# Optimization experiments

Hardware: AMD Instinct MI355X
Metric: run time of the kernel (lower is better)

Reference implementation:

```python
import jax, jax.numpy as jnp
import numpy as np
from jax import lax

C_IN, N_BR, K, H, W_IMG, B = 16, 32, 5, 224, 224, 16
C_SEL = C_IN // 2  # each pattern column selects exactly 8 channels
# circulant connectivity pattern, matches init_kwargs pattern literal
PATTERN = ((np.arange(C_IN)[:, None] + np.arange(N_BR)[None, :]) % C_IN < C_SEL).astype(np.int64)
# np.where returns sorted indices, matching the torch forward's index order
IDX = np.stack([np.where(PATTERN[:, i] == 1)[0] for i in range(N_BR)])  # [N_BR, C_SEL]


def setup_inputs() -> dict:
    key = jax.random.key(0)
    k1, k2, k3 = jax.random.split(key, 3)
    x = jax.random.normal(k1, (B, C_IN, H, W_IMG), dtype=jnp.float32)
    # per-branch conv weights stacked: branch i has Conv2d(8 -> 1, 5x5)
    Wc = jax.random.normal(k2, (N_BR, C_SEL, K, K), dtype=jnp.float32) * 0.05
    bc = jax.random.normal(k3, (N_BR,), dtype=jnp.float32) * 0.05
    return {"x": x, "Wc": Wc, "bc": bc}


def reference(x, Wc, bc):
    # gather the selected channels for every branch: [B, N_BR*C_SEL, H, W]
    x_sel = x[:, IDX.reshape(-1)]
    # all branches at once as a grouped convolution (groups = N_BR, 1 out/group)
    y = lax.conv_general_dilated(
        x_sel, Wc,
        window_strides=(1, 1),
        padding=[(2, 2), (2, 2)],
        feature_group_count=N_BR,
        dimension_numbers=("NCHW", "OIHW", "NCHW"),
    )  # [B, N_BR, H, W]
    return jax.nn.sigmoid(y + bc[None, :, None, None])
```

## Files before the change

kernel.cpp:

```cpp
#include <hip/hip_runtime.h>
#include <math.h>


#define HH 224
#define WW 224
#define BB 16
#define CIN 16
#define NBR 32
#define PH 228
#define PW 228
#define KSTEPS 13

typedef short short8 __attribute__((ext_vector_type(8)));
typedef float f32x4 __attribute__((ext_vector_type(4)));

static __device__ __forceinline__ unsigned short f2bf(float f) {
    unsigned int u = __float_as_uint(f);
    return (unsigned short)((u + 0x7FFFu + ((u >> 16) & 1u)) >> 16);
}

__global__ __launch_bounds__(64)
void prep_wfrag(const float* __restrict__ Wc, short* __restrict__ ws) {
    int t = blockIdx.x * 64 + threadIdx.x;
    int lane = t & 63;
    int rest = t >> 6;
    int nt = rest & 1;
    int kstep = rest >> 1;
    int n = lane & 15;
    int bi = nt * 16 + n;
    int kbase = kstep * 32 + (lane >> 4) * 8;
    short8 pack;
    #pragma unroll
    for (int j = 0; j < 8; ++j) {
        int kg = kbase + j;
        float val = 0.0f;
        if (kg < 400) {
            int tap = kg >> 4;
            int c = kg & 15;
            if (((c + bi) & 15) < 8) {
                int jsel = 0;
                for (int cc = 0; cc < c; ++cc) jsel += (((cc + bi) & 15) < 8) ? 1 : 0;
                val = Wc[(bi * 8 + jsel) * 25 + tap];
            }
        }
        pack[j] = (short)f2bf(val);
    }
    *(short8*)(ws + (size_t)t * 8) = pack;
}

__global__ __launch_bounds__(256)
void transpose_x(const float* __restrict__ x, short* __restrict__ xT) {
    const int b = blockIdx.y;
    const int prow = blockIdx.x * 4 + (threadIdx.x >> 6);
    const int t = threadIdx.x & 63;
    const int gh = prow - 2;
    short* dst = xT + ((size_t)b * PH + prow) * (PW * CIN);

    if (t < 56) {
        const int gw = t * 4;
        unsigned int pk[4][8];
        if ((unsigned)gh < HH) {
            const float* xp = x + (size_t)b * CIN * HH * WW + (size_t)gh * WW + gw;
            #pragma unroll
            for (int w2 = 0; w2 < 8; ++w2) {
                float4 v0 = *(const float4*)(xp + (size_t)(2 * w2) * (HH * WW));
                float4 v1 = *(const float4*)(xp + (size_t)(2 * w2 + 1) * (HH * WW));
                const float* f0 = (const float*)&v0;
                const float* f1 = (const float*)&v1;
                #pragma unroll
                for (int p = 0; p < 4; ++p)
                    pk[p][w2] = (unsigned)f2bf(f0[p]) | ((unsigned)f2bf(f1[p]) << 16);
            }
        } else {
            #pragma unroll
            for (int p = 0; p < 4; ++p)
                #pragma unroll
                for (int w2 = 0; w2 < 8; ++w2) pk[p][w2] = 0u;
        }
        #pragma unroll
        for (int p = 0; p < 4; ++p) {
            int4* o = (int4*)(dst + (size_t)(gw + 2 + p) * CIN);
            o[0] = make_int4(pk[p][0], pk[p][1], pk[p][2], pk[p][3]);
            o[1] = make_int4(pk[p][4], pk[p][5], pk[p][6], pk[p][7]);
        }
    } else if (t == 56) {
        int4 z = make_int4(0, 0, 0, 0);
        int4* o0 = (int4*)(dst);
        o0[0] = z; o0[1] = z;
        int4* o1 = (int4*)(dst + 226 * CIN);
        o1[0] = z; o1[1] = z;
    }
}

__global__ __launch_bounds__(448)
void semiconv_main(const short* __restrict__ xT,
                   const short* __restrict__ wfrag,
                   const float* __restrict__ bc,
                   float* __restrict__ out) {
    __shared__ short tile[5 * PW * CIN];

    const int bidx = blockIdx.x;
    const int b = blockIdx.y;
    const int h = (bidx & 7) * 28 + (bidx >> 3);
    const int tid = threadIdx.x;
    const int wave = tid >> 6;
    const int lane = tid & 63;

    const short* src0 = xT + ((size_t)b * PH + h) * (PW * CIN);
    #pragma unroll
    for (int i = 0; i < 5; ++i) {
        __builtin_amdgcn_global_load_lds(
            (const __attribute__((address_space(1))) void*)(src0 + (size_t)(tid + i * 448) * 8),
            (__attribute__((address_space(3))) void*)(tile + (wave * 64 + i * 448) * 8),
            16, 0, 0);
    }
    if (tid < 40) {
        const int chunk = 2240 + tid;
        *(int4*)(tile + chunk * 8) = *(const int4*)(src0 + (size_t)chunk * 8);
    }
    __syncthreads();

    const int m = lane & 15;
    const int c0 = ((lane >> 4) & 1) * 8;
    const int half = lane >> 5;
    const int wbase = wave * 32;
    const int baseA = (wbase + m) * CIN + c0;

    f32x4 acc[2][2] = {};
    const short8* wfv = (const short8*)wfrag;

    #pragma unroll
    for (int k = 0; k < KSTEPS; ++k) {
        const int tA = 2 * k, tB = 2 * k + 1;
        const int offA = (tA / 5) * (PW * CIN) + (tA % 5) * CIN;
        const int offB = (tB < 25) ? (tB / 5) * (PW * CIN) + (tB % 5) * CIN
                                   : offA;
        const int tapoff = half ? offB : offA;
        short8 b0 = wfv[(k * 2 + 0) * 64 + lane];
        short8 b1 = wfv[(k * 2 + 1) * 64 + lane];
        #pragma unroll
        for (int mt = 0; mt < 2; ++mt) {
            short8 a = *(const short8*)&tile[tapoff + baseA + mt * 16 * CIN];
            acc[mt][0] = __builtin_amdgcn_mfma_f32_16x16x32_bf16(a, b0, acc[mt][0], 0, 0, 0);
            acc[mt][1] = __builtin_amdgcn_mfma_f32_16x16x32_bf16(a, b1, acc[mt][1], 0, 0, 0);
        }
    }

    const int rowm = (lane >> 4) * 4;
    #pragma unroll
    for (int nt = 0; nt < 2; ++nt) {
        const int branch = nt * 16 + m;
        const float bias = bc[branch];
        #pragma unroll
        for (int mt = 0; mt < 2; ++mt) {
            const int w = wbase + mt * 16 + rowm;
            float4 v;
            v.x = __builtin_amdgcn_rcpf(1.0f + __expf(-(acc[mt][nt][0] + bias)));
            v.y = __builtin_amdgcn_rcpf(1.0f + __expf(-(acc[mt][nt][1] + bias)));
            v.z = __builtin_amdgcn_rcpf(1.0f + __expf(-(acc[mt][nt][2] + bias)));
            v.w = __builtin_amdgcn_rcpf(1.0f + __expf(-(acc[mt][nt][3] + bias)));
            *(float4*)(out + (((size_t)b * NBR + branch) * HH + h) * WW + w) = v;
        }
    }
}

extern "C" void kernel_launch(void* const* d_in, const int* in_sizes, int n_in,
                              void* d_out, int out_size, void* d_ws, size_t ws_size,
                              hipStream_t stream) {
    const float* x  = (const float*)d_in[0];
    const float* Wc = (const float*)d_in[1];
    const float* bc = (const float*)d_in[2];
    float* out = (float*)d_out;

    short* wfrag = (short*)d_ws;
    short* xT    = (short*)((char*)d_ws + 32768);

    prep_wfrag<<<26, 64, 0, stream>>>(Wc, wfrag);
    transpose_x<<<dim3(57, 16), 256, 0, stream>>>(x, xT);
    semiconv_main<<<dim3(224, 16), 448, 0, stream>>>(xT, wfrag, bc, out);
}
```

Before: 182.6 us.

## Compute two output rows per block to reuse halo tile and weights

Each block now loads a 6-row halo tile and computes two adjacent output rows, doubling accumulators and halving the grid. This amortizes the halo row loads (6 rows for 2 outputs instead of 5 for 1) and the per-k-step weight fragment loads across twice the MFMA work. It costs more LDS and registers per block and halves the block count, which may lower occupancy and leave the machine less evenly loaded. The launch bound also adds a minimum-blocks hint.

```diff
diff --git a/kernel.cpp b/kernel.cpp
--- a/kernel.cpp
+++ b/kernel.cpp
@@ -92,74 +92,82 @@
     }
 }
 
-__global__ __launch_bounds__(448)
+__global__ __launch_bounds__(448, 4)
 void semiconv_main(const short* __restrict__ xT,
                    const short* __restrict__ wfrag,
                    const float* __restrict__ bc,
                    float* __restrict__ out) {
-    __shared__ short tile[5 * PW * CIN];
+    __shared__ short tile[6 * PW * CIN];
 
     const int bidx = blockIdx.x;
     const int b = blockIdx.y;
-    const int h = (bidx & 7) * 28 + (bidx >> 3);
+    const int h = ((bidx & 7) * 14 + (bidx >> 3)) * 2;
     const int tid = threadIdx.x;
     const int wave = tid >> 6;
     const int lane = tid & 63;
 
     const short* src0 = xT + ((size_t)b * PH + h) * (PW * CIN);
     #pragma unroll
-    for (int i = 0; i < 5; ++i) {
+    for (int i = 0; i < 6; ++i) {
         __builtin_amdgcn_global_load_lds(
             (const __attribute__((address_space(1))) void*)(src0 + (size_t)(tid + i * 448) * 8),
             (__attribute__((address_space(3))) void*)(tile + (wave * 64 + i * 448) * 8),
             16, 0, 0);
     }
-    if (tid < 40) {
-        const int chunk = 2240 + tid;
+    if (tid < 48) {
+        const int chunk = 2688 + tid;
         *(int4*)(tile + chunk * 8) = *(const int4*)(src0 + (size_t)chunk * 8);
     }
     __syncthreads();
 
     const int m = lane & 15;
-    const int c0 = ((lane >> 4) & 1) * 8;
+    const int chalf = (lane >> 4) & 1;
     const int half = lane >> 5;
     const int wbase = wave * 32;
-    const int baseA = (wbase + m) * CIN + c0;
 
-    f32x4 acc[2][2] = {};
+    f32x4 acc[2][2][2] = {};
     const short8* wfv = (const short8*)wfrag;
 
     #pragma unroll
-    for (int k = 0; k < KSTEPS; ++k) {
-        const int tA = 2 * k, tB = 2 * k + 1;
-        const int offA = (tA / 5) * (PW * CIN) + (tA % 5) * CIN;
-        const int offB = (tB < 25) ? (tB / 5) * (PW * CIN) + (tB % 5) * CIN
-                                   : offA;
-        const int tapoff = half ? offB : offA;
-        short8 b0 = wfv[(k * 2 + 0) * 64 + lane];
-        short8 b1 = wfv[(k * 2 + 1) * 64 + lane];
+    for (int s = 0; s < KSTEPS; ++s) {
+        const int t0 = 2 * s;
+        const int t1 = (2 * s + 1 < 25) ? (2 * s + 1) : 24;
+        const int kh0 = t0 / 5, kw0 = t0 % 5;
+        const int kh1 = t1 / 5, kw1 = t1 % 5;
+        const int kh = half ? kh1 : kh0;
+        const int kw = half ? kw1 : kw0;
+        short8 b0 = wfv[(s * 2 + 0) * 64 + lane];
+        short8 b1 = wfv[(s * 2 + 1) * 64 + lane];
         #pragma unroll
-        for (int mt = 0; mt < 2; ++mt) {
-            short8 a = *(const short8*)&tile[tapoff + baseA + mt * 16 * CIN];
-            acc[mt][0] = __builtin_amdgcn_mfma_f32_16x16x32_bf16(a, b0, acc[mt][0], 0, 0, 0);
-            acc[mt][1] = __builtin_amdgcn_mfma_f32_16x16x32_bf16(a, b1, acc[mt][1], 0, 0, 0);
+        for (int r = 0; r < 2; ++r) {
+            const int base = (((r + kh) * PW) + wbase + m + kw) * CIN + chalf * 8;
+            short8 a0 = *(const short8*)&tile[base];
+            short8 a1 = *(const short8*)&tile[base + 16 * CIN];
+            acc[r][0][0] = __builtin_amdgcn_mfma_f32_16x16x32_bf16(a0, b0, acc[r][0][0], 0, 0, 0);
+            acc[r][0][1] = __builtin_amdgcn_mfma_f32_16x16x32_bf16(a0, b1, acc[r][0][1], 0, 0, 0);
+            acc[r][1][0] = __builtin_amdgcn_mfma_f32_16x16x32_bf16(a1, b0, acc[r][1][0], 0, 0, 0);
+            acc[r][1][1] = __builtin_amdgcn_mfma_f32_16x16x32_bf16(a1, b1, acc[r][1][1], 0, 0, 0);
         }
     }
 
     const int rowm = (lane >> 4) * 4;
     #pragma unroll
-    for (int nt = 0; nt < 2; ++nt) {
-        const int branch = nt * 16 + m;
-        const float bias = bc[branch];
+    for (int r = 0; r < 2; ++r) {
+        const int hrow = h + r;
         #pragma unroll
-        for (int mt = 0; mt < 2; ++mt) {
-            const int w = wbase + mt * 16 + rowm;
-            float4 v;
-            v.x = __builtin_amdgcn_rcpf(1.0f + __expf(-(acc[mt][nt][0] + bias)));
-            v.y = __builtin_amdgcn_rcpf(1.0f + __expf(-(acc[mt][nt][1] + bias)));
-            v.z = __builtin_amdgcn_rcpf(1.0f + __expf(-(acc[mt][nt][2] + bias)));
-            v.w = __builtin_amdgcn_rcpf(1.0f + __expf(-(acc[mt][nt][3] + bias)));
-            *(float4*)(out + (((size_t)b * NBR + branch) * HH + h) * WW + w) = v;
+        for (int nt = 0; nt < 2; ++nt) {
+            const int branch = nt * 16 + m;
+            const float bias = bc[branch];
+            #pragma unroll
+            for (int mt = 0; mt < 2; ++mt) {
+                const int w0c = wbase + mt * 16 + rowm;
+                float4 o;
+                o.x = __builtin_amdgcn_rcpf(1.0f + __expf(-(acc[r][mt][nt][0] + bias)));
+                o.y = __builtin_amdgcn_rcpf(1.0f + __expf(-(acc[r][mt][nt][1] + bias)));
+                o.z = __builtin_amdgcn_rcpf(1.0f + __expf(-(acc[r][mt][nt][2] + bias)));
+                o.w = __builtin_amdgcn_rcpf(1.0f + __expf(-(acc[r][mt][nt][3] + bias)));
+                *(float4*)(out + (((size_t)b * NBR + branch) * HH + hrow) * WW + w0c) = o;
+            }
         }
     }
 }
@@ -177,5 +185,5 @@
 
     prep_wfrag<<<26, 64, 0, stream>>>(Wc, wfrag);
     transpose_x<<<dim3(57, 16), 256, 0, stream>>>(x, xT);
-    semiconv_main<<<dim3(224, 16), 448, 0, stream>>>(xT, wfrag, bc, out);
+    semiconv_main<<<dim3(112, 16), 448, 0, stream>>>(xT, wfrag, bc, out);
 }
```

Result: no change. 180.6 us (-1.1%).

## Compute four output rows per block with 32x32x16 MFMA and swizzled LDS layout

Applied to the files above, without the earlier changes.

The main conv kernel now computes a band of four output rows per block instead of one. It loads an 8-row halo tile into LDS and uses 32x32x16 bf16 MFMAs, where M covers 32 pixels and N covers all 32 branches, looping over 25 taps with 16 channels each. This removes the wasted padded K step, and each weight fragment is now reused across four rows. The transposed input layout uses an XOR swizzle of the channel halves to reduce LDS bank conflicts. In exchange the kernel holds 64 accumulator registers per lane and launches fewer, larger blocks (56x16 grid) with launch bounds of 2 blocks.

```diff
diff --git a/kernel.cpp b/kernel.cpp
--- a/kernel.cpp
+++ b/kernel.cpp
@@ -9,10 +9,11 @@
 #define NBR 32
 #define PH 228
 #define PW 228
-#define KSTEPS 13
+#define HW (HH * WW)
+#define UNITS 456
 
 typedef short short8 __attribute__((ext_vector_type(8)));
-typedef float f32x4 __attribute__((ext_vector_type(4)));
+typedef float f32x16 __attribute__((ext_vector_type(16)));
 
 static __device__ __forceinline__ unsigned short f2bf(float f) {
     unsigned int u = __float_as_uint(f);
@@ -20,146 +21,135 @@
 }
 
 __global__ __launch_bounds__(64)
-void prep_wfrag(const float* __restrict__ Wc, short* __restrict__ ws) {
-    int t = blockIdx.x * 64 + threadIdx.x;
-    int lane = t & 63;
-    int rest = t >> 6;
-    int nt = rest & 1;
-    int kstep = rest >> 1;
-    int n = lane & 15;
-    int bi = nt * 16 + n;
-    int kbase = kstep * 32 + (lane >> 4) * 8;
+void prep_wfrag32(const float* __restrict__ Wc, short* __restrict__ ws) {
+    const int tap = blockIdx.x;
+    const int lane = threadIdx.x;
+    const int n = lane & 31;
+    const int cgrp = lane >> 5;
     short8 pack;
     #pragma unroll
     for (int j = 0; j < 8; ++j) {
-        int kg = kbase + j;
+        int c = cgrp * 8 + j;
         float val = 0.0f;
-        if (kg < 400) {
-            int tap = kg >> 4;
-            int c = kg & 15;
-            if (((c + bi) & 15) < 8) {
-                int jsel = 0;
-                for (int cc = 0; cc < c; ++cc) jsel += (((cc + bi) & 15) < 8) ? 1 : 0;
-                val = Wc[(bi * 8 + jsel) * 25 + tap];
-            }
+        if (tap < 25 && (((c + n) & 15) < 8)) {
+            int jsel = 0;
+            for (int cc = 0; cc < c; ++cc) jsel += (((cc + n) & 15) < 8) ? 1 : 0;
+            val = Wc[(n * 8 + jsel) * 25 + tap];
         }
         pack[j] = (short)f2bf(val);
     }
-    *(short8*)(ws + (size_t)t * 8) = pack;
+    *(short8*)(ws + (size_t)(tap * 64 + lane) * 8) = pack;
 }
 
-__global__ __launch_bounds__(256)
+__global__ __launch_bounds__(512)
 void transpose_x(const float* __restrict__ x, short* __restrict__ xT) {
     const int b = blockIdx.y;
-    const int prow = blockIdx.x * 4 + (threadIdx.x >> 6);
-    const int t = threadIdx.x & 63;
+    const int prow = blockIdx.x * 4 + (threadIdx.x >> 7);
+    const int u = threadIdx.x & 127;
     const int gh = prow - 2;
-    short* dst = xT + ((size_t)b * PH + prow) * (PW * CIN);
+    const bool rok = (unsigned)gh < (unsigned)HH;
+    short* dst = xT + ((size_t)b * PH + prow) * (UNITS * 8);
 
-    if (t < 56) {
-        const int gw = t * 4;
-        unsigned int pk[4][8];
-        if ((unsigned)gh < HH) {
-            const float* xp = x + (size_t)b * CIN * HH * WW + (size_t)gh * WW + gw;
+    if (u < 112) {
+        const int t4 = u >> 1;
+        const int sh8 = u & 1;
+        const int gw = t4 * 4;
+        float4 v[8];
+        if (rok) {
+            const float* xp = x + ((size_t)(b * CIN + sh8 * 8) * HH + gh) * WW + gw;
             #pragma unroll
-            for (int w2 = 0; w2 < 8; ++w2) {
-                float4 v0 = *(const float4*)(xp + (size_t)(2 * w2) * (HH * WW));
-                float4 v1 = *(const float4*)(xp + (size_t)(2 * w2 + 1) * (HH * WW));
-                const float* f0 = (const float*)&v0;
-                const float* f1 = (const float*)&v1;
-                #pragma unroll
-                for (int p = 0; p < 4; ++p)
-                    pk[p][w2] = (unsigned)f2bf(f0[p]) | ((unsigned)f2bf(f1[p]) << 16);
-            }
+            for (int i = 0; i < 8; ++i) v[i] = *(const float4*)(xp + (size_t)i * HW);
         } else {
             #pragma unroll
-            for (int p = 0; p < 4; ++p)
-                #pragma unroll
-                for (int w2 = 0; w2 < 8; ++w2) pk[p][w2] = 0u;
+            for (int i = 0; i < 8; ++i) v[i] = make_float4(0.f, 0.f, 0.f, 0.f);
         }
         #pragma unroll
         for (int p = 0; p < 4; ++p) {
-            int4* o = (int4*)(dst + (size_t)(gw + 2 + p) * CIN);
-            o[0] = make_int4(pk[p][0], pk[p][1], pk[p][2], pk[p][3]);
-            o[1] = make_int4(pk[p][4], pk[p][5], pk[p][6], pk[p][7]);
+            const int pcol = gw + 2 + p;
+            const float* f = (const float*)&v[0];
+            int4 pk;
+            pk.x = (int)((unsigned)f2bf(((const float*)&v[0])[p]) | ((unsigned)f2bf(((const float*)&v[1])[p]) << 16));
+            pk.y = (int)((unsigned)f2bf(((const float*)&v[2])[p]) | ((unsigned)f2bf(((const float*)&v[3])[p]) << 16));
+            pk.z = (int)((unsigned)f2bf(((const float*)&v[4])[p]) | ((unsigned)f2bf(((const float*)&v[5])[p]) << 16));
+            pk.w = (int)((unsigned)f2bf(((const float*)&v[6])[p]) | ((unsigned)f2bf(((const float*)&v[7])[p]) << 16));
+            const int unit = pcol * 2 + (sh8 ^ ((pcol >> 2) & 1));
+            *(int4*)(dst + (size_t)unit * 8) = pk;
+            (void)f;
         }
-    } else if (t == 56) {
-        int4 z = make_int4(0, 0, 0, 0);
-        int4* o0 = (int4*)(dst);
-        o0[0] = z; o0[1] = z;
-        int4* o1 = (int4*)(dst + 226 * CIN);
-        o1[0] = z; o1[1] = z;
+    } else if (u == 112) {
+        const int4 z = make_int4(0, 0, 0, 0);
+        #pragma unroll
+        for (int i = 0; i < 4; ++i) {
+            const int pcol = (i < 2) ? i : 224 + i;
+            *(int4*)(dst + (size_t)(pcol * 2 + 0) * 8) = z;
+            *(int4*)(dst + (size_t)(pcol * 2 + 1) * 8) = z;
+        }
     }
 }
 
-__global__ __launch_bounds__(448)
+__global__ __launch_bounds__(448, 2)
 void semiconv_main(const short* __restrict__ xT,
                    const short* __restrict__ wfrag,
                    const float* __restrict__ bc,
                    float* __restrict__ out) {
-    __shared__ short tile[5 * PW * CIN];
+    __shared__ short tile[8 * UNITS * 8];
 
     const int bidx = blockIdx.x;
     const int b = blockIdx.y;
-    const int h = (bidx & 7) * 28 + (bidx >> 3);
+    const int band = (bidx & 7) * 7 + (bidx >> 3);
+    const int h = band * 4;
     const int tid = threadIdx.x;
     const int wave = tid >> 6;
     const int lane = tid & 63;
 
-    const short* src0 = xT + ((size_t)b * PH + h) * (PW * CIN);
+    const short* src0 = xT + ((size_t)b * PH + h) * (UNITS * 8);
     #pragma unroll
-    for (int i = 0; i < 5; ++i) {
+    for (int i = 0; i < 8; ++i) {
         __builtin_amdgcn_global_load_lds(
             (const __attribute__((address_space(1))) void*)(src0 + (size_t)(tid + i * 448) * 8),
             (__attribute__((address_space(3))) void*)(tile + (wave * 64 + i * 448) * 8),
             16, 0, 0);
     }
-    if (tid < 40) {
-        const int chunk = 2240 + tid;
+    if (tid < 64) {
+        const int chunk = 3584 + tid;
         *(int4*)(tile + chunk * 8) = *(const int4*)(src0 + (size_t)chunk * 8);
     }
     __syncthreads();
 
-    const int m = lane & 15;
-    const int c0 = ((lane >> 4) & 1) * 8;
-    const int half = lane >> 5;
+    const int l31 = lane & 31;
+    const int chalf = lane >> 5;
     const int wbase = wave * 32;
-    const int baseA = (wbase + m) * CIN + c0;
 
-    f32x4 acc[2][2] = {};
+    f32x16 acc[4] = {};
     const short8* wfv = (const short8*)wfrag;
 
     #pragma unroll
-    for (int k = 0; k < KSTEPS; ++k) {
-        const int tA = 2 * k, tB = 2 * k + 1;
-        const int offA = (tA / 5) * (PW * CIN) + (tA % 5) * CIN;
-        const int offB = (tB < 25) ? (tB / 5) * (PW * CIN) + (tB % 5) * CIN
-                                   : offA;
-        const int tapoff = half ? offB : offA;
-        short8 b0 = wfv[(k * 2 + 0) * 64 + lane];
-        short8 b1 = wfv[(k * 2 + 1) * 64 + lane];
+    for (int s = 0; s < 25; ++s) {
+        const int kh = s / 5, kw = s % 5;
+        const short8 bfr = wfv[s * 64 + lane];
+        const int px = wbase + l31 + kw;
+        const int ubase = px * 2 + (chalf ^ ((px >> 2) & 1));
         #pragma unroll
-        for (int mt = 0; mt < 2; ++mt) {
-            short8 a = *(const short8*)&tile[tapoff + baseA + mt * 16 * CIN];
-            acc[mt][0] = __builtin_amdgcn_mfma_f32_16x16x32_bf16(a, b0, acc[mt][0], 0, 0, 0);
-            acc[mt][1] = __builtin_amdgcn_mfma_f32_16x16x32_bf16(a, b1, acc[mt][1], 0, 0, 0);
+        for (int r = 0; r < 4; ++r) {
+            const short8 a = *(const short8*)&tile[(size_t)((r + kh) * UNITS + ubase) * 8];
+            acc[r] = __builtin_amdgcn_mfma_f32_32x32x16_bf16(a, bfr, acc[r], 0, 0, 0);
         }
     }
 
-    const int rowm = (lane >> 4) * 4;
+    const float bias = bc[l31];
     #pragma unroll
-    for (int nt = 0; nt < 2; ++nt) {
-        const int branch = nt * 16 + m;
-        const float bias = bc[branch];
+    for (int r = 0; r < 4; ++r) {
+        const int hrow = h + r;
+        float* orow = out + (((size_t)b * NBR + l31) * HH + hrow) * WW;
         #pragma unroll
-        for (int mt = 0; mt < 2; ++mt) {
-            const int w = wbase + mt * 16 + rowm;
-            float4 v;
-            v.x = __builtin_amdgcn_rcpf(1.0f + __expf(-(acc[mt][nt][0] + bias)));
-            v.y = __builtin_amdgcn_rcpf(1.0f + __expf(-(acc[mt][nt][1] + bias)));
-            v.z = __builtin_amdgcn_rcpf(1.0f + __expf(-(acc[mt][nt][2] + bias)));
-            v.w = __builtin_amdgcn_rcpf(1.0f + __expf(-(acc[mt][nt][3] + bias)));
-            *(float4*)(out + (((size_t)b * NBR + branch) * HH + h) * WW + w) = v;
+        for (int q = 0; q < 4; ++q) {
+            const int w0c = wbase + q * 8 + chalf * 4;
+            float4 o;
+            o.x = __builtin_amdgcn_rcpf(1.0f + __expf(-(acc[r][q * 4 + 0] + bias)));
+            o.y = __builtin_amdgcn_rcpf(1.0f + __expf(-(acc[r][q * 4 + 1] + bias)));
+            o.z = __builtin_amdgcn_rcpf(1.0f + __expf(-(acc[r][q * 4 + 2] + bias)));
+            o.w = __builtin_amdgcn_rcpf(1.0f + __expf(-(acc[r][q * 4 + 3] + bias)));
+            *(float4*)(orow + w0c) = o;
         }
     }
 }
@@ -175,7 +165,7 @@
     short* wfrag = (short*)d_ws;
     short* xT    = (short*)((char*)d_ws + 32768);
 
-    prep_wfrag<<<26, 64, 0, stream>>>(Wc, wfrag);
-    transpose_x<<<dim3(57, 16), 256, 0, stream>>>(x, xT);
-    semiconv_main<<<dim3(224, 16), 448, 0, stream>>>(xT, wfrag, bc, out);
+    prep_wfrag32<<<26, 64, 0, stream>>>(Wc, wfrag);
+    transpose_x<<<dim3(57, 16), 512, 0, stream>>>(x, xT);
+    semiconv_main<<<dim3(56, 16), 448, 0, stream>>>(xT, wfrag, bc, out);
 }
```

Result: no change. 183.9 us (+0.7%).
